# Optimization experiments

Hardware: AMD Instinct MI355X
Metric: run time of the kernel (lower is better)

Reference implementation:

```python
import jax, jax.numpy as jnp
import numpy as np

D = 1024      # n_embd
H = 2048      # expert_hidden_dim
G = 4         # num_groups
EPG = 2       # experts_per_group
NH = 16       # num_heads
HD = D // NH  # head dim
L = 4         # num_layers
V = 32000     # vocab_size
NC = 32000    # num_classes
MAXS = 2048   # max_seq_len
B, S = 2, 1024
TEMP = 1.0    # router_temperature


def setup_inputs() -> dict:
    key = jax.random.key(0)
    ks = jax.random.split(key, 12)
    sc = 0.02
    def n(k, shape):
        return jax.random.normal(k, shape, jnp.float32) * sc
    return {
        "x": jax.random.randint(ks[0], (B, S), 0, V),
        "tok_emb": n(ks[1], (V, D)),
        "pos_emb": n(ks[2], (MAXS, D)),
        "in_proj_w": n(ks[3], (L, 3 * D, D)),
        "in_proj_b": jnp.zeros((L, 3 * D)),
        "out_w": n(ks[4], (L, D, D)),
        "out_b": jnp.zeros((L, D)),
        "ln1_w": jnp.ones((L, D)), "ln1_b": jnp.zeros((L, D)),
        "ln2_w": jnp.ones((L, D)), "ln2_b": jnp.zeros((L, D)),
        "gr_w": n(ks[5], (L, D, G)), "gr_b": jnp.zeros((L, G)),
        "er_w": n(ks[6], (L, G, D, EPG)), "er_b": jnp.zeros((L, G, EPG)),
        "w1": n(ks[7], (L, G, EPG, D, H)), "b1": jnp.zeros((L, G, EPG, H)),
        "w2": n(ks[8], (L, G, EPG, H, D)), "b2": jnp.zeros((L, G, EPG, D)),
        "lnf_w": jnp.ones((D,)), "lnf_b": jnp.zeros((D,)),
        "head_w": n(ks[9], (NC, D)), "head_b": jnp.zeros((NC,)),
    }


def _ln(x, w, b):
    m = x.mean(-1, keepdims=True)
    v = ((x - m) ** 2).mean(-1, keepdims=True)
    return (x - m) * jax.lax.rsqrt(v + 1e-5) * w + b


def _attn(x, wqkv, bqkv, wo, bo, mask):
    b, s, _ = x.shape
    qkv = x @ wqkv.T + bqkv
    q, k, v = jnp.split(qkv, 3, axis=-1)
    def heads(t):
        return t.reshape(b, s, NH, HD).transpose(0, 2, 1, 3)
    q, k, v = heads(q), heads(k), heads(v)
    sc = jnp.einsum('bhqd,bhkd->bhqk', q, k) / np.float32(np.sqrt(HD))
    sc = jnp.where(mask, sc, jnp.float32(-1e30))
    a = jax.nn.softmax(sc, axis=-1)
    o = jnp.einsum('bhqk,bhkd->bhqd', a, v).transpose(0, 2, 1, 3).reshape(b, s, D)
    return o @ wo.T + bo


def _moe(x, gw, gb, ew, eb, w1, b1, w2, b2):
    # x: [T, D] flattened tokens. 2-level routing: top-1 group, top-1 expert in group.
    gp = jax.nn.softmax((x @ gw + gb) / TEMP, axis=-1)                      # [T,G]
    gidx = jnp.argmax(gp, axis=-1)                                          # [T]
    ep = jax.nn.softmax((jnp.einsum('td,gde->tge', x, ew) + eb) / TEMP, -1)  # [T,G,EPG]
    ep_sel = jnp.take_along_axis(ep, gidx[:, None, None], axis=1)[:, 0]     # [T,EPG]
    eidx = jnp.argmax(ep_sel, axis=-1)                                      # [T]
    gate = (jnp.take_along_axis(gp, gidx[:, None], 1)[:, 0]
            * jnp.take_along_axis(ep_sel, eidx[:, None], 1)[:, 0])          # [T]
    hmid = jax.nn.relu(jnp.einsum('td,gedh->tgeh', x, w1) + b1)             # [T,G,EPG,H]
    out = jnp.einsum('tgeh,gehd->tged', hmid, w2) + b2                      # [T,G,EPG,D]
    comb = (jax.nn.one_hot(gidx, G, dtype=x.dtype)[:, :, None]
            * jax.nn.one_hot(eidx, EPG, dtype=x.dtype)[:, None, :]) * gate[:, None, None]
    return jnp.einsum('tge,tged->td', comb, out)


def reference(x, tok_emb, pos_emb, in_proj_w, in_proj_b, out_w, out_b,
              ln1_w, ln1_b, ln2_w, ln2_b, gr_w, gr_b, er_w, er_b,
              w1, b1, w2, b2, lnf_w, lnf_b, head_w, head_b):
    b, s = x.shape
    h = tok_emb[x] + pos_emb[jnp.arange(s)][None]
    mask = jnp.tril(jnp.ones((s, s), bool))
    for l in range(L):
        x1 = _ln(h, ln1_w[l], ln1_b[l])
        h = h + _attn(x1, in_proj_w[l], in_proj_b[l], out_w[l], out_b[l], mask)
        x2 = _ln(h, ln2_w[l], ln2_b[l]).reshape(b * s, D)
        h = h + _moe(x2, gr_w[l], gr_b[l], er_w[l], er_b[l],
                     w1[l], b1[l], w2[l], b2[l]).reshape(b, s, D)
    h = _ln(h, lnf_w, lnf_b).mean(axis=1)
    return h @ head_w.T + head_b
```

## Files before the change

kernel.cpp:

```cpp
#include <hip/hip_runtime.h>
#include <hip/hip_bf16.h>
#include <cstdint>
#include <cstddef>

#define D_   1024
#define H_   2048
#define G_   4
#define EPG_ 2
#define NE_  8
#define NH_  16
#define HD_  64
#define L_   4
#define V_   32000
#define NC_  32000
#define B_   2
#define S_   1024
#define T_   2048
#define MAXBLK_ 24
#define QB_  128

typedef __attribute__((__ext_vector_type__(8))) __bf16 bf16x8;
typedef __attribute__((__ext_vector_type__(4))) __bf16 bf16x4;
typedef __attribute__((__ext_vector_type__(4))) float  f32x4;

__device__ __forceinline__ void gl_lds16(const void* g, void* l) {
  __builtin_amdgcn_global_load_lds(
      (const __attribute__((address_space(1))) void*)g,
      (__attribute__((address_space(3))) void*)l, 16, 0, 0);
}

__device__ __forceinline__ float wave_sum(float v) {
  #pragma unroll
  for (int o = 32; o >= 1; o >>= 1) v += __shfl_xor(v, o, 64);
  return v;
}

__global__ __launch_bounds__(256) void embed_kernel(const int* __restrict__ x,
    const float* __restrict__ tok, const float* __restrict__ pos,
    float* __restrict__ h) {
  int t = blockIdx.x;
  int tid = threadIdx.x;
  int token = x[t];
  int s = t & (S_ - 1);
  float4 tv = *(const float4*)(tok + (size_t)token * D_ + tid * 4);
  float4 pv = *(const float4*)(pos + (size_t)s * D_ + tid * 4);
  float4 r;
  r.x = tv.x + pv.x; r.y = tv.y + pv.y; r.z = tv.z + pv.z; r.w = tv.w + pv.w;
  *(float4*)(h + (size_t)t * D_ + tid * 4) = r;
}

__device__ __forceinline__ float block_sum256(float v, float* sbuf) {
  v = wave_sum(v);
  int tid = threadIdx.x;
  if ((tid & 63) == 0) sbuf[tid >> 6] = v;
  __syncthreads();
  float r = sbuf[0] + sbuf[1] + sbuf[2] + sbuf[3];
  __syncthreads();
  return r;
}

template<bool F32OUT, bool BFOUT>
__global__ __launch_bounds__(256) void ln_kernel(const float* __restrict__ X,
    const float* __restrict__ w, const float* __restrict__ b,
    float* __restrict__ Yf, __bf16* __restrict__ Yb) {
  __shared__ float sbuf[4];
  int t = blockIdx.x, tid = threadIdx.x;
  const float* xr = X + (size_t)t * D_;
  float4 v = *(const float4*)(xr + tid * 4);
  float sum = v.x + v.y + v.z + v.w;
  float m = block_sum256(sum, sbuf) * (1.0f / D_);
  float dx = v.x - m, dy = v.y - m, dz = v.z - m, dw = v.w - m;
  float vs = dx * dx + dy * dy + dz * dz + dw * dw;
  float var = block_sum256(vs, sbuf) * (1.0f / D_);
  float rs = rsqrtf(var + 1e-5f);
  float4 wv = *(const float4*)(w + tid * 4);
  float4 bv = *(const float4*)(b + tid * 4);
  float4 o;
  o.x = dx * rs * wv.x + bv.x;
  o.y = dy * rs * wv.y + bv.y;
  o.z = dz * rs * wv.z + bv.z;
  o.w = dw * rs * wv.w + bv.w;
  if (F32OUT) *(float4*)(Yf + (size_t)t * D_ + tid * 4) = o;
  if (BFOUT) {
    bf16x4 ob = {(__bf16)o.x, (__bf16)o.y, (__bf16)o.z, (__bf16)o.w};
    *(bf16x4*)(Yb + (size_t)t * D_ + tid * 4) = ob;
  }
}

__global__ __launch_bounds__(256) void ln_route_kernel(const float* __restrict__ X,
    const float* __restrict__ lw, const float* __restrict__ lb,
    const float* __restrict__ gw, const float* __restrict__ gb,
    const float* __restrict__ ew, const float* __restrict__ eb,
    __bf16* __restrict__ Yb, int* __restrict__ eidx, float* __restrict__ gate) {
  int wv = threadIdx.x >> 6, lane = threadIdx.x & 63;
  int t = blockIdx.x * 4 + wv;
  const float* xr = X + (size_t)t * D_;
  float4 xv[4];
  #pragma unroll
  for (int k = 0; k < 4; k++) xv[k] = *(const float4*)(xr + lane * 4 + k * 256);
  float s = 0.f;
  #pragma unroll
  for (int k = 0; k < 4; k++) s += xv[k].x + xv[k].y + xv[k].z + xv[k].w;
  float m = wave_sum(s) * (1.0f / D_);
  float vs = 0.f;
  #pragma unroll
  for (int k = 0; k < 4; k++) {
    float a = xv[k].x - m, b2 = xv[k].y - m, c = xv[k].z - m, d = xv[k].w - m;
    vs += a * a + b2 * b2 + c * c + d * d;
  }
  float rs = rsqrtf(wave_sum(vs) * (1.0f / D_) + 1e-5f);
  float y[4][4];
  #pragma unroll
  for (int k = 0; k < 4; k++) {
    int d0 = lane * 4 + k * 256;
    float4 wv4 = *(const float4*)(lw + d0);
    float4 bv4 = *(const float4*)(lb + d0);
    y[k][0] = (xv[k].x - m) * rs * wv4.x + bv4.x;
    y[k][1] = (xv[k].y - m) * rs * wv4.y + bv4.y;
    y[k][2] = (xv[k].z - m) * rs * wv4.z + bv4.z;
    y[k][3] = (xv[k].w - m) * rs * wv4.w + bv4.w;
    bf16x4 ob = {(__bf16)y[k][0], (__bf16)y[k][1], (__bf16)y[k][2], (__bf16)y[k][3]};
    *(bf16x4*)(Yb + (size_t)t * D_ + d0) = ob;
  }
  float g0 = 0, g1 = 0, g2 = 0, g3 = 0;
  #pragma unroll
  for (int k = 0; k < 4; k++)
    #pragma unroll
    for (int j = 0; j < 4; j++) {
      int d = lane * 4 + k * 256 + j;
      float4 gv = *(const float4*)(gw + (size_t)d * G_);
      float yv = y[k][j];
      g0 += yv * gv.x; g1 += yv * gv.y; g2 += yv * gv.z; g3 += yv * gv.w;
    }
  g0 = wave_sum(g0) + gb[0];
  g1 = wave_sum(g1) + gb[1];
  g2 = wave_sum(g2) + gb[2];
  g3 = wave_sum(g3) + gb[3];
  float mx = fmaxf(fmaxf(g0, g1), fmaxf(g2, g3));
  float p0 = __expf(g0 - mx), p1 = __expf(g1 - mx), p2 = __expf(g2 - mx), p3 = __expf(g3 - mx);
  float psum = p0 + p1 + p2 + p3;
  int gidx = 0; float best = g0;
  if (g1 > best) { best = g1; gidx = 1; }
  if (g2 > best) { best = g2; gidx = 2; }
  if (g3 > best) { best = g3; gidx = 3; }
  float gpsel = ((gidx == 0) ? p0 : (gidx == 1) ? p1 : (gidx == 2) ? p2 : p3) / psum;
  const float* ewg = ew + (size_t)gidx * D_ * EPG_;
  float e0 = 0, e1 = 0;
  #pragma unroll
  for (int k = 0; k < 4; k++)
    #pragma unroll
    for (int j = 0; j < 4; j++) {
      int d = lane * 4 + k * 256 + j;
      float2 ev = *(const float2*)(ewg + (size_t)d * EPG_);
      e0 += y[k][j] * ev.x; e1 += y[k][j] * ev.y;
    }
  e0 = wave_sum(e0) + eb[gidx * EPG_ + 0];
  e1 = wave_sum(e1) + eb[gidx * EPG_ + 1];
  float em = fmaxf(e0, e1);
  float q0 = __expf(e0 - em), q1 = __expf(e1 - em);
  int ei = (e1 > e0) ? 1 : 0;
  float epsel = ((ei == 0) ? q0 : q1) / (q0 + q1);
  if (lane == 0) {
    eidx[t] = gidx * EPG_ + ei;
    gate[t] = gpsel * epsel;
  }
}

__global__ __launch_bounds__(256) void finalize_kernel(const int* __restrict__ eidx,
    int* __restrict__ counts, int* __restrict__ offs, int* __restrict__ tlist,
    int* __restrict__ blk) {
  __shared__ int hist[256][NE_];
  __shared__ int eoff[NE_];
  int tid = threadIdx.x;
  int loc[NE_];
  #pragma unroll
  for (int e = 0; e < NE_; e++) loc[e] = 0;
  int te[8];
  #pragma unroll
  for (int i = 0; i < 8; i++) { te[i] = eidx[tid * 8 + i]; loc[te[i]]++; }
  #pragma unroll
  for (int e = 0; e < NE_; e++) hist[tid][e] = loc[e];
  __syncthreads();
  for (int off = 1; off < 256; off <<= 1) {
    int v[NE_];
    #pragma unroll
    for (int e = 0; e < NE_; e++) v[e] = (tid >= off) ? hist[tid - off][e] : 0;
    __syncthreads();
    #pragma unroll
    for (int e = 0; e < NE_; e++) hist[tid][e] += v[e];
    __syncthreads();
  }
  if (tid == 0) {
    int acc = 0, nb = 0;
    for (int e = 0; e < NE_; e++) {
      int c = hist[255][e];
      eoff[e] = acc; counts[e] = c; offs[e] = acc; acc += c;
      for (int mt = 0; mt * 128 < c; mt++) blk[nb++] = e | (mt << 8);
    }
    for (; nb < MAXBLK_; nb++) blk[nb] = -1;
  }
  __syncthreads();
  int run[NE_];
  #pragma unroll
  for (int e = 0; e < NE_; e++) run[e] = eoff[e] + hist[tid][e] - loc[e];
  #pragma unroll
  for (int i = 0; i < 8; i++) {
    int e = te[i];
    tlist[run[e]++] = tid * 8 + i;
  }
}

template<int MODE, int NF, bool KN>
__global__ __launch_bounds__(256, 2) void gemm_mfma(
    const __bf16* __restrict__ A, const float* __restrict__ W,
    const float* __restrict__ bias, float* __restrict__ Cf,
    __bf16* __restrict__ Cb, const int* __restrict__ tlist,
    const int* __restrict__ offs, const int* __restrict__ counts,
    const float* __restrict__ gate, const int* __restrict__ blk,
    int N, int K) {
  __shared__ __bf16 As[128 * 64];
  __shared__ __bf16 Bs[NF * 32 * 64];
  int e = 0, mt = blockIdx.y, cnt = T_;
  if (MODE >= 2) {
    int bv = blk[blockIdx.y];
    if (bv < 0) return;
    e = bv & 255; mt = bv >> 8;
    cnt = counts[e];
  }
  int row0 = mt * 128;
  int lbase = (MODE >= 2) ? offs[e] : 0;
  int col0 = blockIdx.x * (NF * 32);
  const float* Wp = W + (size_t)e * N * K;
  const float* bp = bias + (size_t)e * N;
  int tid = threadIdx.x;
  int w = tid >> 6, lane = tid & 63, lq = lane & 15, lg = lane >> 4;
  int wr = w >> 1, wc = w & 1;

  const __bf16* asrc[4];
  #pragma unroll
  for (int it = 0; it < 4; it++) {
    int v = it * 256 + tid;
    int r = v >> 3, u = v & 7;
    int gr = row0 + r;
    long rowidx;
    if (MODE == 2) rowidx = tlist[lbase + ((gr < cnt) ? gr : cnt - 1)];
    else if (MODE == 3) rowidx = lbase + ((gr < cnt) ? gr : cnt - 1);
    else rowidx = gr;
    asrc[it] = A + (size_t)rowidx * K + (u ^ (r & 7)) * 8;
  }
  const float* bsrc[NF];
  int bdst[NF];
  #pragma unroll
  for (int it = 0; it < NF; it++) {
    if (!KN) {
      int v = it * 256 + tid;
      int n = v >> 3, u = v & 7;
      bsrc[it] = Wp + (size_t)(col0 + n) * K + u * 8;
      bdst[it] = n * 64 + (u ^ (n & 7)) * 8;
    } else {
      int v = it * 256 + tid;
      int n = v & (NF * 32 - 1), u = v / (NF * 32);
      bsrc[it] = Wp + (size_t)(u * 8) * N + col0 + n;
      bdst[it] = n * 64 + (u ^ (n & 7)) * 8;
    }
  }

  float br0[NF * 8], br1[NF * 8];
  f32x4 acc[4][NF] = {};

  auto loadB = [&](float* br, int k0) {
    #pragma unroll
    for (int it = 0; it < NF; it++) {
      if (!KN) {
        float4 f0 = *(const float4*)(bsrc[it] + k0);
        float4 f1 = *(const float4*)(bsrc[it] + k0 + 4);
        br[it * 8 + 0] = f0.x; br[it * 8 + 1] = f0.y;
        br[it * 8 + 2] = f0.z; br[it * 8 + 3] = f0.w;
        br[it * 8 + 4] = f1.x; br[it * 8 + 5] = f1.y;
        br[it * 8 + 6] = f1.z; br[it * 8 + 7] = f1.w;
      } else {
        #pragma unroll
        for (int j = 0; j < 8; j++)
          br[it * 8 + j] = bsrc[it][(size_t)(k0 + j) * N];
      }
    }
  };
  auto writeB = [&](const float* br) {
    #pragma unroll
    for (int it = 0; it < NF; it++) {
      bf16x8 bb = {(__bf16)br[it * 8 + 0], (__bf16)br[it * 8 + 1],
                   (__bf16)br[it * 8 + 2], (__bf16)br[it * 8 + 3],
                   (__bf16)br[it * 8 + 4], (__bf16)br[it * 8 + 5],
                   (__bf16)br[it * 8 + 6], (__bf16)br[it * 8 + 7]};
      *(bf16x8*)&Bs[bdst[it]] = bb;
    }
  };
  auto stageA = [&](int k0) {
    #pragma unroll
    for (int it = 0; it < 4; it++)
      gl_lds16(asrc[it] + k0, &As[(it * 256 + tid) * 8]);
  };
  auto mfmaPhase = [&]() {
    #pragma unroll
    for (int kk = 0; kk < 2; kk++) {
      bf16x8 a[4], b[NF];
      int us = ((lg + kk * 4) ^ (lq & 7)) * 8;
      #pragma unroll
      for (int fi = 0; fi < 4; fi++)
        a[fi] = *(const bf16x8*)&As[(wr * 64 + fi * 16 + lq) * 64 + us];
      #pragma unroll
      for (int fj = 0; fj < NF; fj++)
        b[fj] = *(const bf16x8*)&Bs[(wc * (NF * 16) + fj * 16 + lq) * 64 + us];
      #pragma unroll
      for (int fi = 0; fi < 4; fi++)
        #pragma unroll
        for (int fj = 0; fj < NF; fj++)
          acc[fi][fj] = __builtin_amdgcn_mfma_f32_16x16x32_bf16(a[fi], b[fj], acc[fi][fj], 0, 0, 0);
    }
  };

  loadB(br0, 0);
  for (int k0 = 0; k0 < K; k0 += 128) {
    stageA(k0);
    writeB(br0);
    loadB(br1, k0 + 64);
    __syncthreads();
    mfmaPhase();
    __syncthreads();
    stageA(k0 + 64);
    writeB(br1);
    if (k0 + 128 < K) loadB(br0, k0 + 128);
    __syncthreads();
    mfmaPhase();
    __syncthreads();
  }

  #pragma unroll
  for (int fi = 0; fi < 4; fi++) {
    #pragma unroll
    for (int v = 0; v < 4; v++) {
      int r = row0 + wr * 64 + fi * 16 + lg * 4 + v;
      long orow;
      float gv = 1.f;
      if (MODE >= 2) {
        if (r >= cnt) continue;
        if (MODE == 2) orow = lbase + r;
        else { orow = tlist[lbase + r]; gv = gate[orow]; }
      } else {
        orow = r;
      }
      #pragma unroll
      for (int fj = 0; fj < NF; fj++) {
        int c = col0 + wc * (NF * 16) + fj * 16 + lq;
        float val = acc[fi][fj][v] + bp[c];
        if (MODE == 0)      Cb[orow * N + c] = (__bf16)val;
        else if (MODE == 1) Cf[orow * N + c] += val;
        else if (MODE == 2) Cb[orow * N + c] = (__bf16)fmaxf(val, 0.f);
        else                Cf[orow * N + c] += gv * val;
      }
    }
  }
}

#define SC_LOG2 0.18033688011112042f
__global__ __launch_bounds__(512) void attn_mfma_kernel(const __bf16* __restrict__ qkv,
                                                        __bf16* __restrict__ out) {
  __shared__ __bf16 Ks[64][72];
  __shared__ __bf16 Vt[64][72];
  __shared__ __bf16 Ps[QB_][72];
  int tid = threadIdx.x;
  int w = tid >> 6, lane = tid & 63, lq = lane & 15, lg = lane >> 4;
  int qt = (S_ / QB_ - 1) - blockIdx.x;
  int b = blockIdx.y >> 4, hh = blockIdx.y & 15;
  const __bf16* qbase = qkv + (size_t)b * S_ * 3 * D_ + hh * HD_;

  bf16x8 qa[2];
  {
    const __bf16* qp = qbase + (size_t)(qt * QB_ + w * 16 + lq) * 3 * D_ + lg * 8;
    qa[0] = *(const bf16x8*)qp;
    qa[1] = *(const bf16x8*)(qp + 32);
  }

  f32x4 o[4] = {};
  float m_[4] = {-1e30f, -1e30f, -1e30f, -1e30f};
  float l_[4] = {0.f, 0.f, 0.f, 0.f};

  int rowmin = qt * QB_ + w * 16;
  int srow = tid >> 3, sc8 = tid & 7;
  int nkt = qt * 2 + 2;

  for (int kt = 0; kt < nkt; kt++) {
    {
      const __bf16* kp = qbase + (size_t)(kt * 64 + srow) * 3 * D_ + D_ + sc8 * 8;
      *(bf16x8*)&Ks[srow][sc8 * 8] = *(const bf16x8*)kp;
      bf16x8 vv = *(const bf16x8*)(kp + D_);
      int cs = srow ^ (sc8 << 3);
      #pragma unroll
      for (int j = 0; j < 8; j++) Vt[sc8 * 8 + j][cs] = vv[j];
    }
    __syncthreads();

    if (kt * 64 <= rowmin + 15) {
      f32x4 s[4] = {};
      #pragma unroll
      for (int kk = 0; kk < 2; kk++)
        #pragma unroll
        for (int fc = 0; fc < 4; fc++) {
          bf16x8 kf = *(const bf16x8*)&Ks[fc * 16 + lq][lg * 8 + kk * 32];
          s[fc] = __builtin_amdgcn_mfma_f32_16x16x32_bf16(qa[kk], kf, s[fc], 0, 0, 0);
        }

      bool need_mask = (kt * 64 + 63 > rowmin);
      #pragma unroll
      for (int fc = 0; fc < 4; fc++)
        #pragma unroll
        for (int v = 0; v < 4; v++) {
          float sv = s[fc][v] * SC_LOG2;
          if (need_mask && (kt * 64 + fc * 16 + lq) > (rowmin + lg * 4 + v)) sv = -1e30f;
          s[fc][v] = sv;
        }

      #pragma unroll
      for (int v = 0; v < 4; v++) {
        float rm = fmaxf(fmaxf(s[0][v], s[1][v]), fmaxf(s[2][v], s[3][v]));
        #pragma unroll
        for (int o2 = 8; o2 >= 1; o2 >>= 1) rm = fmaxf(rm, __shfl_xor(rm, o2, 64));
        if (rm > m_[v]) {
          float cc = exp2f(m_[v] - rm);
          m_[v] = rm;
          l_[v] *= cc;
          o[0][v] *= cc; o[1][v] *= cc; o[2][v] *= cc; o[3][v] *= cc;
        }
        float rs = 0.f;
        #pragma unroll
        for (int fc = 0; fc < 4; fc++) {
          float p = exp2f(s[fc][v] - m_[v]);
          s[fc][v] = p; rs += p;
        }
        l_[v] += rs;
        #pragma unroll
        for (int fc = 0; fc < 4; fc++)
          Ps[w * 16 + lg * 4 + v][fc * 16 + lq] = (__bf16)s[fc][v];
      }
      asm volatile("" ::: "memory");

      #pragma unroll
      for (int kk = 0; kk < 2; kk++) {
        bf16x8 pa = *(const bf16x8*)&Ps[w * 16 + lq][lg * 8 + kk * 32];
        #pragma unroll
        for (int dc = 0; dc < 4; dc++) {
          int d = dc * 16 + lq;
          int col = (lg * 8 + kk * 32) ^ ((d >> 3) << 3);
          bf16x8 vb = *(const bf16x8*)&Vt[d][col];
          o[dc] = __builtin_amdgcn_mfma_f32_16x16x32_bf16(pa, vb, o[dc], 0, 0, 0);
        }
      }
    }
    __syncthreads();
  }

  #pragma unroll
  for (int v = 0; v < 4; v++) {
    float ls = l_[v];
    #pragma unroll
    for (int o2 = 8; o2 >= 1; o2 >>= 1) ls += __shfl_xor(ls, o2, 64);
    float inv = 1.0f / ls;
    int row = rowmin + lg * 4 + v;
    __bf16* op = out + ((size_t)b * S_ + row) * D_ + hh * HD_;
    #pragma unroll
    for (int dc = 0; dc < 4; dc++)
      op[dc * 16 + lq] = (__bf16)(o[dc][v] * inv);
  }
}

__global__ __launch_bounds__(256) void mean_part_kernel(const float* __restrict__ X,
                                                        float* __restrict__ part) {
  int bd = blockIdx.x * 256 + threadIdx.x;
  int chunk = blockIdx.y;
  int b = bd >> 10, d = bd & 1023;
  float s = 0.f;
  #pragma unroll 4
  for (int i = 0; i < 64; i++) {
    int sidx = chunk * 64 + i;
    s += X[((size_t)b * S_ + sidx) * D_ + d];
  }
  part[chunk * T_ + bd] = s;
}

__global__ __launch_bounds__(256) void mean_final_kernel(const float* __restrict__ part,
                                                         float* __restrict__ hm) {
  int bd = blockIdx.x * 256 + threadIdx.x;
  float s = 0.f;
  #pragma unroll
  for (int c = 0; c < 16; c++) s += part[c * T_ + bd];
  hm[bd] = s * (1.0f / S_);
}

__global__ __launch_bounds__(256) void head_kernel(const float* __restrict__ hm,
    const float* __restrict__ hw, const float* __restrict__ hb,
    float* __restrict__ out) {
  int w = threadIdx.x >> 6;
  int lane = threadIdx.x & 63;
  int c = blockIdx.x * 4 + w;
  const float* row = hw + (size_t)c * D_;
  float acc0 = 0.f, acc1 = 0.f;
  #pragma unroll
  for (int k = 0; k < 4; k++) {
    int d = lane * 4 + k * 256;
    float4 wv = *(const float4*)(row + d);
    float4 h0 = *(const float4*)(hm + d);
    float4 h1 = *(const float4*)(hm + D_ + d);
    acc0 += wv.x * h0.x + wv.y * h0.y + wv.z * h0.z + wv.w * h0.w;
    acc1 += wv.x * h1.x + wv.y * h1.y + wv.z * h1.z + wv.w * h1.w;
  }
  #pragma unroll
  for (int o = 32; o >= 1; o >>= 1) {
    acc0 += __shfl_xor(acc0, o, 64);
    acc1 += __shfl_xor(acc1, o, 64);
  }
  if (lane == 0) {
    float bias = hb[c];
    out[c] = acc0 + bias;
    out[NC_ + c] = acc1 + bias;
  }
}

extern "C" void kernel_launch(void* const* d_in, const int* in_sizes, int n_in,
                              void* d_out, int out_size, void* d_ws, size_t ws_size,
                              hipStream_t stream) {
  const int*   x        = (const int*)d_in[0];
  const float* tok_emb  = (const float*)d_in[1];
  const float* pos_emb  = (const float*)d_in[2];
  const float* in_proj_w= (const float*)d_in[3];
  const float* in_proj_b= (const float*)d_in[4];
  const float* out_w    = (const float*)d_in[5];
  const float* out_b    = (const float*)d_in[6];
  const float* ln1_w    = (const float*)d_in[7];
  const float* ln1_b    = (const float*)d_in[8];
  const float* ln2_w    = (const float*)d_in[9];
  const float* ln2_b    = (const float*)d_in[10];
  const float* gr_w     = (const float*)d_in[11];
  const float* gr_b     = (const float*)d_in[12];
  const float* er_w     = (const float*)d_in[13];
  const float* er_b     = (const float*)d_in[14];
  const float* w1       = (const float*)d_in[15];
  const float* b1       = (const float*)d_in[16];
  const float* w2       = (const float*)d_in[17];
  const float* b2       = (const float*)d_in[18];
  const float* lnf_w    = (const float*)d_in[19];
  const float* lnf_b    = (const float*)d_in[20];
  const float* head_w   = (const float*)d_in[21];
  const float* head_b   = (const float*)d_in[22];

  char* wp = (char*)d_ws;
  auto carve = [&](size_t bytes) -> char* {
    char* p = wp;
    wp += (bytes + 255) & ~(size_t)255;
    return p;
  };
  float*  h      = (float*)carve((size_t)T_ * D_ * 4);
  float*  x1     = (float*)carve((size_t)T_ * D_ * 4);
  __bf16* x1b    = (__bf16*)carve((size_t)T_ * D_ * 2);
  __bf16* qkvb   = (__bf16*)carve((size_t)T_ * 3 * D_ * 2);
  __bf16* attnb  = (__bf16*)carve((size_t)T_ * D_ * 2);
  __bf16* hmidb  = (__bf16*)carve((size_t)T_ * H_ * 2);
  float*  part   = (float*)carve((size_t)16 * T_ * 4);
  float*  hm     = (float*)carve((size_t)B_ * D_ * 4);
  float*  gate   = (float*)carve((size_t)T_ * 4);
  int*    eidx   = (int*)carve((size_t)T_ * 4);
  int*    tlist  = (int*)carve((size_t)T_ * 4);
  int*    counts = (int*)carve(64);
  int*    offs   = (int*)carve(64);
  int*    blk    = (int*)carve(MAXBLK_ * 4);

  embed_kernel<<<T_, 256, 0, stream>>>(x, tok_emb, pos_emb, h);

  for (int l = 0; l < L_; l++) {
    ln_kernel<false, true><<<T_, 256, 0, stream>>>(h, ln1_w + l * D_, ln1_b + l * D_,
                                                   nullptr, x1b);
    gemm_mfma<0, 4, false><<<dim3(24, 16, 1), 256, 0, stream>>>(
        x1b, in_proj_w + (size_t)l * 3 * D_ * D_, in_proj_b + (size_t)l * 3 * D_,
        nullptr, qkvb, nullptr, nullptr, nullptr, nullptr, nullptr, 3 * D_, D_);
    attn_mfma_kernel<<<dim3(S_ / QB_, B_ * NH_), 512, 0, stream>>>(qkvb, attnb);
    gemm_mfma<1, 2, false><<<dim3(16, 16, 1), 256, 0, stream>>>(
        attnb, out_w + (size_t)l * D_ * D_, out_b + (size_t)l * D_, h, nullptr,
        nullptr, nullptr, nullptr, nullptr, nullptr, D_, D_);

    ln_route_kernel<<<T_ / 4, 256, 0, stream>>>(h,
        ln2_w + l * D_, ln2_b + l * D_,
        gr_w + (size_t)l * D_ * G_, gr_b + (size_t)l * G_,
        er_w + (size_t)l * G_ * D_ * EPG_, er_b + (size_t)l * G_ * EPG_,
        x1b, eidx, gate);
    finalize_kernel<<<1, 256, 0, stream>>>(eidx, counts, offs, tlist, blk);

    gemm_mfma<2, 4, true><<<dim3(H_ / 128, MAXBLK_, 1), 256, 0, stream>>>(
        x1b, w1 + (size_t)l * NE_ * D_ * H_, b1 + (size_t)l * NE_ * H_, nullptr, hmidb,
        tlist, offs, counts, nullptr, blk, H_, D_);
    gemm_mfma<3, 2, true><<<dim3(D_ / 64, MAXBLK_, 1), 256, 0, stream>>>(
        hmidb, w2 + (size_t)l * NE_ * H_ * D_, b2 + (size_t)l * NE_ * D_, h, nullptr,
        tlist, offs, counts, gate, blk, D_, H_);
  }

  ln_kernel<true, false><<<T_, 256, 0, stream>>>(h, lnf_w, lnf_b, x1, nullptr);
  mean_part_kernel<<<dim3(B_ * D_ / 256, 16), 256, 0, stream>>>(x1, part);
  mean_final_kernel<<<B_ * D_ / 256, 256, 0, stream>>>(part, hm);
  head_kernel<<<NC_ / 4, 256, 0, stream>>>(hm, head_w, head_b, (float*)d_out);
}
```

Before: 888.2 us.

## Double-buffer LDS tiles in MFMA GEMM and raise wave priority during MFMA

The GEMM mainloop now keeps two LDS buffers for the A and B tiles. Each iteration prefetches the next K-slice (async A copy plus B register load) while running MFMA on the current buffer, and needs one barrier per 64-wide K step instead of two. It also raises wave priority around the MFMA phase with s_setprio. The cost is twice the shared memory per block, which may lower occupancy under launch_bounds(256,2), and B values staying live in registers across the MFMA phase.

```diff
diff --git a/kernel.cpp b/kernel.cpp
--- a/kernel.cpp
+++ b/kernel.cpp
@@ -218,8 +218,8 @@
     const int* __restrict__ offs, const int* __restrict__ counts,
     const float* __restrict__ gate, const int* __restrict__ blk,
     int N, int K) {
-  __shared__ __bf16 As[128 * 64];
-  __shared__ __bf16 Bs[NF * 32 * 64];
+  __shared__ __bf16 As[2][128 * 64];
+  __shared__ __bf16 Bs[2][NF * 32 * 64];
   int e = 0, mt = blockIdx.y, cnt = T_;
   if (MODE >= 2) {
     int bv = blk[blockIdx.y];
@@ -265,74 +265,78 @@
     }
   }
 
-  float br0[NF * 8], br1[NF * 8];
+  float brp[NF * 8];
   f32x4 acc[4][NF] = {};
 
-  auto loadB = [&](float* br, int k0) {
+  auto loadB = [&](int k0) {
     #pragma unroll
     for (int it = 0; it < NF; it++) {
       if (!KN) {
         float4 f0 = *(const float4*)(bsrc[it] + k0);
         float4 f1 = *(const float4*)(bsrc[it] + k0 + 4);
-        br[it * 8 + 0] = f0.x; br[it * 8 + 1] = f0.y;
-        br[it * 8 + 2] = f0.z; br[it * 8 + 3] = f0.w;
-        br[it * 8 + 4] = f1.x; br[it * 8 + 5] = f1.y;
-        br[it * 8 + 6] = f1.z; br[it * 8 + 7] = f1.w;
+        brp[it * 8 + 0] = f0.x; brp[it * 8 + 1] = f0.y;
+        brp[it * 8 + 2] = f0.z; brp[it * 8 + 3] = f0.w;
+        brp[it * 8 + 4] = f1.x; brp[it * 8 + 5] = f1.y;
+        brp[it * 8 + 6] = f1.z; brp[it * 8 + 7] = f1.w;
       } else {
         #pragma unroll
         for (int j = 0; j < 8; j++)
-          br[it * 8 + j] = bsrc[it][(size_t)(k0 + j) * N];
+          brp[it * 8 + j] = bsrc[it][(size_t)(k0 + j) * N];
       }
     }
   };
-  auto writeB = [&](const float* br) {
+  auto writeB = [&](int buf) {
     #pragma unroll
     for (int it = 0; it < NF; it++) {
-      bf16x8 bb = {(__bf16)br[it * 8 + 0], (__bf16)br[it * 8 + 1],
-                   (__bf16)br[it * 8 + 2], (__bf16)br[it * 8 + 3],
-                   (__bf16)br[it * 8 + 4], (__bf16)br[it * 8 + 5],
-                   (__bf16)br[it * 8 + 6], (__bf16)br[it * 8 + 7]};
-      *(bf16x8*)&Bs[bdst[it]] = bb;
+      bf16x8 bb = {(__bf16)brp[it * 8 + 0], (__bf16)brp[it * 8 + 1],
+                   (__bf16)brp[it * 8 + 2], (__bf16)brp[it * 8 + 3],
+                   (__bf16)brp[it * 8 + 4], (__bf16)brp[it * 8 + 5],
+                   (__bf16)brp[it * 8 + 6], (__bf16)brp[it * 8 + 7]};
+      *(bf16x8*)&Bs[buf][bdst[it]] = bb;
     }
   };
-  auto stageA = [&](int k0) {
+  auto stageA = [&](int buf, int k0) {
     #pragma unroll
     for (int it = 0; it < 4; it++)
-      gl_lds16(asrc[it] + k0, &As[(it * 256 + tid) * 8]);
+      gl_lds16(asrc[it] + k0, &As[buf][(it * 256 + tid) * 8]);
   };
-  auto mfmaPhase = [&]() {
+  auto mfmaPhase = [&](int buf) {
+    __builtin_amdgcn_s_setprio(1);
     #pragma unroll
     for (int kk = 0; kk < 2; kk++) {
       bf16x8 a[4], b[NF];
       int us = ((lg + kk * 4) ^ (lq & 7)) * 8;
       #pragma unroll
       for (int fi = 0; fi < 4; fi++)
-        a[fi] = *(const bf16x8*)&As[(wr * 64 + fi * 16 + lq) * 64 + us];
+        a[fi] = *(const bf16x8*)&As[buf][(wr * 64 + fi * 16 + lq) * 64 + us];
       #pragma unroll
       for (int fj = 0; fj < NF; fj++)
-        b[fj] = *(const bf16x8*)&Bs[(wc * (NF * 16) + fj * 16 + lq) * 64 + us];
+        b[fj] = *(const bf16x8*)&Bs[buf][(wc * (NF * 16) + fj * 16 + lq) * 64 + us];
       #pragma unroll
       for (int fi = 0; fi < 4; fi++)
         #pragma unroll
         for (int fj = 0; fj < NF; fj++)
           acc[fi][fj] = __builtin_amdgcn_mfma_f32_16x16x32_bf16(a[fi], b[fj], acc[fi][fj], 0, 0, 0);
     }
+    __builtin_amdgcn_s_setprio(0);
   };
 
-  loadB(br0, 0);
-  for (int k0 = 0; k0 < K; k0 += 128) {
-    stageA(k0);
-    writeB(br0);
-    loadB(br1, k0 + 64);
+  loadB(0);
+  stageA(0, 0);
+  writeB(0);
+  __syncthreads();
+
+  int buf = 0;
+  for (int k0 = 0; k0 < K; k0 += 64) {
+    int nk = k0 + 64;
+    if (nk < K) {
+      stageA(buf ^ 1, nk);
+      loadB(nk);
+    }
+    mfmaPhase(buf);
+    if (nk < K) writeB(buf ^ 1);
     __syncthreads();
-    mfmaPhase();
-    __syncthreads();
-    stageA(k0 + 64);
-    writeB(br1);
-    if (k0 + 128 < K) loadB(br0, k0 + 128);
-    __syncthreads();
-    mfmaPhase();
-    __syncthreads();
+    buf ^= 1;
   }
 
   #pragma unroll
```

Measured after the change: 888.7 us. Within noise of the previous version (+0.1%).
